# Kernel tuning notes

Hardware: AMD Instinct MI355X
Metric: run time of the kernel (lower is better)

The kernel has to match this reference:

```python
import jax, jax.numpy as jnp
import numpy as np

H, NH, R = 128, 8, 6
NB = 2                  # geometric interaction blocks
BS, L, K = 16, 64, 16   # graphs, blocks/graph, atoms/block
NBLK = BS * L           # 1024 blocks total
N = NBLK * K            # 16384 atoms
E = 262144              # atom-level edges
EB = 512                # block-level edges per graph
CUTOFF = 8.0


def _mha(x, in_w, in_b, out_w, out_b):
    # torch nn.MultiheadAttention (batch_first, eval / no dropout). x: [B,S,H]
    B_, S, _ = x.shape
    qkv = x @ in_w + in_b                     # [B,S,3H]
    q, k, v = jnp.split(qkv, 3, axis=-1)
    dh = H // NH
    q = q.reshape(B_, S, NH, dh)
    k = k.reshape(B_, S, NH, dh)
    v = v.reshape(B_, S, NH, dh)
    scores = jnp.einsum('bind,bjnd->bnij', q, k) / np.sqrt(dh).astype(np.float32)
    attn = jax.nn.softmax(scores, axis=-1)
    o = jnp.einsum('bnij,bjnd->bind', attn, v).reshape(B_, S, H)
    return o @ out_w + out_b


def _forward(A, atom_positions, B_types, coords, edge_index, block_edges,
             emb_atom, emb_pos, emb_block, rbf_freq,
             inter_w1, inter_b1, inter_w2, inter_b2,
             upd_w1, upd_b1, upd_w2, upd_b2,
             edge_w1, edge_b1, edge_w2, edge_b2,
             attn_in_w, attn_in_b, attn_out_w, attn_out_b,
             ln_g, ln_b, fin_w1, fin_b1, fin_w2, fin_b2, fin_w3, fin_b3):
    block_id = jnp.repeat(jnp.arange(NBLK), K)  # uniform K atoms per block
    # atom embedding + position embedding + broadcast block embedding
    x = emb_atom[A] + emb_pos[atom_positions] + emb_block[B_types][block_id]  # [N,H]

    # ---- GeometricAtomProcessor ----
    i, j = edge_index[0], edge_index[1]
    d = jnp.linalg.norm(coords[i] - coords[j], axis=-1)       # [E]
    u = jnp.clip(d / CUTOFF, 1e-3, None)
    # DimeNet envelope, exponent=5 -> p=6: 1/u + a u^5 + b u^6 + c u^7
    env = 1.0 / u - 28.0 * u**5 + 48.0 * u**6 - 21.0 * u**7
    rbf = env[:, None] * jnp.sin(rbf_freq[None, :] * u[:, None])  # [E,R]

    for b in range(NB):
        ef = jnp.concatenate([x[i], x[j], rbf], axis=-1)       # [E,2H+R] gather
        m = jax.nn.silu(ef @ inter_w1[b] + inter_b1[b]) @ inter_w2[b] + inter_b2[b]
        agg = jax.ops.segment_sum(m, i, num_segments=N)        # index_add_ scatter
        ui = jnp.concatenate([x, agg], axis=-1)
        x = jax.nn.silu(ui @ upd_w1[b] + upd_b1[b]) @ upd_w2[b] + upd_b2[b] + x

    # scatter_mean over block_id (uniform blocks -> reshape mean)
    blocks = x.reshape(NBLK, K, H).mean(axis=1).reshape(BS, L, H)

    # ---- per-graph block-edge attention (batched over graphs) ----
    src, dst = block_edges[..., 0], block_edges[..., 1]        # [BS,EB]
    bidx = jnp.arange(BS)[:, None]
    ef = jnp.concatenate([blocks[bidx, src], blocks[bidx, dst]], axis=-1)  # [BS,EB,2H]
    ef = jax.nn.relu(ef @ edge_w1 + edge_b1) @ edge_w2 + edge_b2
    ea = _mha(ef, attn_in_w, attn_in_b, attn_out_w, attn_out_b)            # [BS,EB,H]
    seg = (src + bidx * L).reshape(-1)
    sums = jax.ops.segment_sum(ea.reshape(-1, H), seg, num_segments=NBLK)
    cnt = jax.ops.segment_sum(jnp.ones((BS * EB,), ea.dtype), seg, num_segments=NBLK)
    blocks = blocks + (sums / jnp.maximum(cnt, 1.0)[:, None]).reshape(BS, L, H)

    # ---- block self-attention + mean pool ----
    att = _mha(blocks, attn_in_w, attn_in_b, attn_out_w, attn_out_b)
    g = att.mean(axis=1)                                       # [BS,H]
    mu = g.mean(-1, keepdims=True)
    var = ((g - mu) ** 2).mean(-1, keepdims=True)
    g = (g - mu) / jnp.sqrt(var + 1e-5) * ln_g + ln_b
    h1 = jax.nn.relu(g @ fin_w1 + fin_b1)
    h2 = jax.nn.relu(h1 @ fin_w2 + fin_b2)
    return (h2 @ fin_w3 + fin_b3).squeeze(-1)                  # [BS]


def setup_inputs() -> dict:
    key = jax.random.key(0)
    ks = jax.random.split(key, 40)
    def nrm(k, shape, s=0.05):
        return jax.random.normal(k, shape, jnp.float32) * s
    inp = {}
    inp['A'] = jax.random.randint(ks[0], (N,), 0, 100)
    inp['atom_positions'] = jax.random.randint(ks[1], (N,), 0, 16)
    inp['B_types'] = jax.random.randint(ks[2], (NBLK,), 0, 1000)
    inp['coords'] = jax.random.uniform(ks[3], (N, 3), jnp.float32, 0.0, 20.0)
    inp['edge_index'] = jax.random.randint(ks[4], (2, E), 0, N)
    inp['block_edges'] = jax.random.randint(ks[5], (BS, EB, 2), 0, L)
    inp['emb_atom'] = nrm(ks[6], (100, H), 0.5)
    inp['emb_pos'] = nrm(ks[7], (16, H), 0.5)
    inp['emb_block'] = nrm(ks[8], (1000, H), 0.5)
    inp['rbf_freq'] = (jnp.arange(1, R + 1, dtype=jnp.float32) * np.pi)
    inp['inter_w1'] = nrm(ks[9], (NB, 2 * H + R, H))
    inp['inter_b1'] = jnp.zeros((NB, H), jnp.float32)
    inp['inter_w2'] = nrm(ks[10], (NB, H, H))
    inp['inter_b2'] = jnp.zeros((NB, H), jnp.float32)
    inp['upd_w1'] = nrm(ks[11], (NB, 2 * H, H))
    inp['upd_b1'] = jnp.zeros((NB, H), jnp.float32)
    inp['upd_w2'] = nrm(ks[12], (NB, H, H))
    inp['upd_b2'] = jnp.zeros((NB, H), jnp.float32)
    inp['edge_w1'] = nrm(ks[13], (2 * H, H))
    inp['edge_b1'] = jnp.zeros((H,), jnp.float32)
    inp['edge_w2'] = nrm(ks[14], (H, H))
    inp['edge_b2'] = jnp.zeros((H,), jnp.float32)
    inp['attn_in_w'] = nrm(ks[15], (H, 3 * H))
    inp['attn_in_b'] = jnp.zeros((3 * H,), jnp.float32)
    inp['attn_out_w'] = nrm(ks[16], (H, H))
    inp['attn_out_b'] = jnp.zeros((H,), jnp.float32)
    inp['ln_g'] = jnp.ones((H,), jnp.float32)
    inp['ln_b'] = jnp.zeros((H,), jnp.float32)
    inp['fin_w1'] = nrm(ks[17], (H, H))
    inp['fin_b1'] = jnp.zeros((H,), jnp.float32)
    inp['fin_w2'] = nrm(ks[18], (H, H))
    inp['fin_b2'] = jnp.zeros((H,), jnp.float32)
    inp['fin_w3'] = nrm(ks[19], (H, 1))
    inp['fin_b3'] = jnp.zeros((1,), jnp.float32)
    return inp


def reference(A, atom_positions, B_types, coords, edge_index, block_edges,
              emb_atom, emb_pos, emb_block, rbf_freq,
              inter_w1, inter_b1, inter_w2, inter_b2,
              upd_w1, upd_b1, upd_w2, upd_b2,
              edge_w1, edge_b1, edge_w2, edge_b2,
              attn_in_w, attn_in_b, attn_out_w, attn_out_b,
              ln_g, ln_b, fin_w1, fin_b1, fin_w2, fin_b2, fin_w3, fin_b3):
    return _forward(A, atom_positions, B_types, coords, edge_index, block_edges,
                    emb_atom, emb_pos, emb_block, rbf_freq,
                    inter_w1, inter_b1, inter_w2, inter_b2,
                    upd_w1, upd_b1, upd_w2, upd_b2,
                    edge_w1, edge_b1, edge_w2, edge_b2,
                    attn_in_w, attn_in_b, attn_out_w, attn_out_b,
                    ln_g, ln_b, fin_w1, fin_b1, fin_w2, fin_b2, fin_w3, fin_b3)
```

## Files before the change

kernel.cpp:

```cpp
#include <hip/hip_runtime.h>
#include <math.h>

#define H 128
#define NHD 8
#define DH 16
#define RB 6
#define NBI 2
#define BSG 16
#define LBLK 64
#define KATOM 16
#define NBLKT 1024
#define NA 16384
#define NE 262144
#define EBE 512

__device__ __forceinline__ float fsilu(float v) {
  return v * __builtin_amdgcn_rcpf(1.0f + __expf(-v));
}

typedef short v4s __attribute__((ext_vector_type(4)));
typedef float f32x4 __attribute__((ext_vector_type(4)));

__device__ __forceinline__ short f2bf(float f) {
  union { float f; unsigned u; } v; v.f = f;
  unsigned r = v.u + 0x7fffu + ((v.u >> 16) & 1u);
  return (short)(r >> 16);
}

__device__ __forceinline__ float bf2f(short s) {
  union { unsigned u; float f; } v;
  v.u = ((unsigned)(unsigned short)s) << 16;
  return v.f;
}

#if defined(__has_builtin)
#if __has_builtin(__builtin_amdgcn_mfma_f32_16x16x16bf16_1k)
#define HAVE_MFMA16_1K 1
#endif
#endif

#ifdef HAVE_MFMA16_1K
__device__ __forceinline__ f32x4 mfma16(v4s a, v4s b, f32x4 c) {
  return __builtin_amdgcn_mfma_f32_16x16x16bf16_1k(a, b, c, 0, 0, 0);
}
#else
typedef short v8s __attribute__((ext_vector_type(8)));
__device__ __forceinline__ f32x4 mfma16(v4s a, v4s b, f32x4 c) {
  v8s a8 = {a[0], a[1], a[2], a[3], 0, 0, 0, 0};
  v8s b8 = {b[0], b[1], b[2], b[3], 0, 0, 0, 0};
  return __builtin_amdgcn_mfma_f32_16x16x32_bf16(a8, b8, c, 0, 0, 0);
}
#endif

__global__ __launch_bounds__(256) void k_embed(
    const int* __restrict__ A, const int* __restrict__ apos,
    const int* __restrict__ btypes,
    const float* __restrict__ emb_atom, const float* __restrict__ emb_pos,
    const float* __restrict__ emb_block, float* __restrict__ x)
{
  int idx = blockIdx.x * 256 + threadIdx.x;
  int n = idx >> 7, h = idx & 127;
  x[idx] = emb_atom[A[n] * H + h] + emb_pos[apos[n] * H + h]
         + emb_block[btypes[n >> 4] * H + h];
}

__global__ __launch_bounds__(256) void k_hist(
    const int* __restrict__ ei, int* __restrict__ cnt)
{
  int e = blockIdx.x * 256 + threadIdx.x;
  atomicAdd(&cnt[ei[e]], 1);
}

__global__ __launch_bounds__(1024) void k_scan(
    const int* __restrict__ cnt, int* __restrict__ off,
    int* __restrict__ cur, float* __restrict__ cntf)
{
  __shared__ int ps[1024];
  int t = threadIdx.x;
  int base = t * 16;
  int local[16];
  int s = 0;
  #pragma unroll
  for (int k = 0; k < 16; ++k) { local[k] = s; s += cnt[base + k]; }
  ps[t] = s;
  __syncthreads();
  for (int d = 1; d < 1024; d <<= 1) {
    int v = (t >= d) ? ps[t - d] : 0;
    __syncthreads();
    ps[t] += v;
    __syncthreads();
  }
  int offset = (t == 0) ? 0 : ps[t - 1];
  #pragma unroll
  for (int k = 0; k < 16; ++k) {
    int o = offset + local[k];
    off[base + k] = o;
    cur[base + k] = o;
    cntf[base + k] = (float)cnt[base + k];
  }
  if (t == 1023) off[NA] = offset + s;
}

__global__ __launch_bounds__(256) void k_scatter(
    const int* __restrict__ ei, const int* __restrict__ ej,
    const float* __restrict__ coords, const float* __restrict__ freq,
    int* __restrict__ cur, int* __restrict__ ej_s, float* __restrict__ rbf_s)
{
  int e = blockIdx.x * 256 + threadIdx.x;
  int i = ei[e], j = ej[e];
  int pos = atomicAdd(&cur[i], 1);
  ej_s[pos] = j;
  float dx = coords[i*3+0] - coords[j*3+0];
  float dy = coords[i*3+1] - coords[j*3+1];
  float dz = coords[i*3+2] - coords[j*3+2];
  float d = sqrtf(dx*dx + dy*dy + dz*dz);
  float u = fmaxf(d * 0.125f, 1e-3f);
  float u2 = u*u, u4 = u2*u2, u5 = u4*u, u6 = u5*u, u7 = u6*u;
  float env = 1.0f/u - 28.0f*u5 + 48.0f*u6 - 21.0f*u7;
  #pragma unroll
  for (int r = 0; r < RB; ++r)
    rbf_s[(size_t)pos*RB + r] = env * __sinf(freq[r] * u);
}

__global__ __launch_bounds__(256) void k_bedge_csr(
    const int* __restrict__ bedges, int* __restrict__ blist,
    int* __restrict__ boff, float* __restrict__ ind)
{
  __shared__ int hist[64], offs[65], curs[64];
  int b = blockIdx.x, t = threadIdx.x;
  if (t < 64) hist[t] = 0;
  __syncthreads();
  for (int e = t; e < EBE; e += 256) atomicAdd(&hist[bedges[(b*EBE + e)*2]], 1);
  __syncthreads();
  if (t == 0) {
    offs[0] = 0;
    for (int k = 0; k < 64; ++k) offs[k+1] = offs[k] + hist[k];
  }
  __syncthreads();
  if (t < 64) curs[t] = offs[t];
  __syncthreads();
  for (int e = t; e < EBE; e += 256) {
    int src = bedges[(b*EBE + e)*2];
    int pos = atomicAdd(&curs[src], 1);
    blist[b*EBE + pos] = e;
  }
  if (t < 65) boff[b*65 + t] = offs[t];
  if (t < 64) ind[b*64 + t] = (hist[t] > 0) ? 1.0f : 0.0f;
}

__global__ __launch_bounds__(256) void k_edge_csr(
    const short* __restrict__ P, const short* __restrict__ Q,
    const float* __restrict__ rbf_s, const float* __restrict__ W1c,
    const int* __restrict__ ej_s, const int* __restrict__ off,
    float* __restrict__ Hagg)
{
  __shared__ float w[RB * H];
  for (int idx = threadIdx.x; idx < RB * H; idx += 256) w[idx] = W1c[idx];
  __syncthreads();
  int c4 = threadIdx.x & 31;
  int sub = threadIdx.x >> 5;
  int i = blockIdx.x * 8 + sub;
  int e0 = off[i], e1 = off[i + 1];
  short4 p4 = *(const short4*)&P[(size_t)i * H + c4 * 4];
  float4 pv = { bf2f(p4.x), bf2f(p4.y), bf2f(p4.z), bf2f(p4.w) };
  float4 W0 = *(const float4*)&w[0*H + c4*4];
  float4 W1 = *(const float4*)&w[1*H + c4*4];
  float4 W2 = *(const float4*)&w[2*H + c4*4];
  float4 W3 = *(const float4*)&w[3*H + c4*4];
  float4 W4 = *(const float4*)&w[4*H + c4*4];
  float4 W5 = *(const float4*)&w[5*H + c4*4];
  float4 acc = {0, 0, 0, 0};
  for (int e = e0; e < e1; ++e) {
    int j = ej_s[e];
    short4 q4 = *(const short4*)&Q[(size_t)j * H + c4 * 4];
    float4 qv = { bf2f(q4.x), bf2f(q4.y), bf2f(q4.z), bf2f(q4.w) };
    const float* rb = &rbf_s[(size_t)e * RB];
    float r0 = rb[0], r1 = rb[1], r2 = rb[2], r3 = rb[3], r4 = rb[4], r5 = rb[5];
    float4 v;
    v.x = pv.x + qv.x + r0*W0.x + r1*W1.x + r2*W2.x + r3*W3.x + r4*W4.x + r5*W5.x;
    v.y = pv.y + qv.y + r0*W0.y + r1*W1.y + r2*W2.y + r3*W3.y + r4*W4.y + r5*W5.y;
    v.z = pv.z + qv.z + r0*W0.z + r1*W1.z + r2*W2.z + r3*W3.z + r4*W4.z + r5*W5.z;
    v.w = pv.w + qv.w + r0*W0.w + r1*W1.w + r2*W2.w + r3*W3.w + r4*W4.w + r5*W5.w;
    acc.x += fsilu(v.x);
    acc.y += fsilu(v.y);
    acc.z += fsilu(v.z);
    acc.w += fsilu(v.w);
  }
  *(float4*)&Hagg[(size_t)i * H + c4 * 4] = acc;
}

__global__ __launch_bounds__(128) void k_wprep(
    const float* __restrict__ W2base, const float* __restrict__ U1base,
    const float* __restrict__ b2base, float* __restrict__ bvecbase,
    short* __restrict__ wt_u1base)
{
  int y = blockIdx.y;
  const float* W2 = W2base + (size_t)y * H * H;
  const float* U1 = U1base + (size_t)y * 2 * H * H;
  const float* b2 = b2base + y * H;
  float* bvec = bvecbase + y * H;
  short* wt1 = wt_u1base + (size_t)y * 128 * 256;
  int k = blockIdx.x, c = threadIdx.x;
  const float* U1b = U1 + 128 * H;
  wt1[c * 256 + k] = f2bf(U1[k * H + c]);
  float s = 0.0f;
  for (int t = 0; t < H; ++t) s += W2[k * H + t] * U1b[t * H + c];
  wt1[c * 256 + 128 + k] = f2bf(s);
  if (k == 0) {
    float sb = 0.0f;
    for (int t = 0; t < H; ++t) sb += b2[t] * U1b[t * H + c];
    bvec[c] = sb;
  }
}

__global__ __launch_bounds__(256) void k_tcvt(
    const float* __restrict__ inter_w1, const float* __restrict__ upd_w2,
    const float* __restrict__ edge_w1, const float* __restrict__ edge_w2,
    const float* __restrict__ attn_in_w,
    short* __restrict__ wt_pq, short* __restrict__ wt_u2,
    short* __restrict__ wt_e1, short* __restrict__ wt_e2,
    short* __restrict__ wt_in)
{
  int idx = blockIdx.x * 256 + threadIdx.x;
  {
    int k = idx & 127, col = (idx >> 7) & 127, y = (idx >> 14) & 1, b = idx >> 15;
    wt_pq[idx] = f2bf(inter_w1[((size_t)b*262 + y*128 + k)*128 + col]);
  }
  if (idx < 2*128*128) {
    int k = idx & 127, col = (idx >> 7) & 127, b = idx >> 14;
    wt_u2[idx] = f2bf(upd_w2[((size_t)b*128 + k)*128 + col]);
    wt_e1[idx] = f2bf(edge_w1[((size_t)b*128 + k)*128 + col]);
  }
  if (idx < 128*128) {
    int k = idx & 127, col = idx >> 7;
    wt_e2[idx] = f2bf(edge_w2[(size_t)k*128 + col]);
  }
  if (idx < 384*128) {
    int k = idx & 127, col = idx >> 7;
    wt_in[idx] = f2bf(attn_in_w[(size_t)k*384 + col]);
  }
}

__global__ __launch_bounds__(256) void k_pq_mfma(
    const float* __restrict__ x, const short* __restrict__ WtPQ,
    const float* __restrict__ b1,
    short* __restrict__ P, short* __restrict__ Q)
{
  __shared__ short As[64][136];
  __shared__ short Ws[128][72];
  int tid = threadIdx.x;
  int m0 = blockIdx.x * 64;
  int y = blockIdx.y;
  const short* Wt = WtPQ + (size_t)y * 128 * 128;
  short* C = y ? Q : P;
  for (int idx = tid; idx < 64*32; idx += 256) {
    int r = idx >> 5, c4 = idx & 31;
    float4 v = *(const float4*)&x[(size_t)(m0 + r)*H + c4*4];
    short4 s4 = { f2bf(v.x), f2bf(v.y), f2bf(v.z), f2bf(v.w) };
    *(short4*)&As[r][c4*4] = s4;
  }
  int lane = tid & 63, wv = tid >> 6;
  int c = lane & 15, g = lane >> 4;
  int rowb = wv * 16;
  f32x4 acc[8];
  #pragma unroll
  for (int t = 0; t < 8; ++t) acc[t] = (f32x4){0,0,0,0};
  for (int kc = 0; kc < 2; ++kc) {
    __syncthreads();
    {
      int col = tid >> 1, hh = (tid & 1) * 32;
      const int4* src = (const int4*)&Wt[col*128 + kc*64 + hh];
      int4 a0 = src[0], a1 = src[1], a2 = src[2], a3 = src[3];
      *(int4*)&Ws[col][hh] = a0;      *(int4*)&Ws[col][hh+8] = a1;
      *(int4*)&Ws[col][hh+16] = a2;   *(int4*)&Ws[col][hh+24] = a3;
    }
    __syncthreads();
    #pragma unroll
    for (int ks = 0; ks < 4; ++ks) {
      v4s a = *(const v4s*)&As[rowb + c][kc*64 + ks*16 + g*4];
      #pragma unroll
      for (int ct = 0; ct < 8; ++ct) {
        v4s bf = *(const v4s*)&Ws[ct*16 + c][ks*16 + g*4];
        acc[ct] = mfma16(a, bf, acc[ct]);
      }
    }
  }
  #pragma unroll
  for (int ct = 0; ct < 8; ++ct) {
    int col = ct*16 + c;
    float bb = y ? 0.0f : b1[col];
    #pragma unroll
    for (int r = 0; r < 4; ++r) {
      int row = m0 + rowb + g*4 + r;
      C[(size_t)row*H + col] = f2bf(acc[ct][r] + bb);
    }
  }
}

__global__ __launch_bounds__(256) void k_upd_mfma(
    const float* __restrict__ x, const float* __restrict__ Hagg,
    const short* __restrict__ Wt1,
    const float* __restrict__ b1, const float* __restrict__ bvec,
    const float* __restrict__ cntf,
    const short* __restrict__ Wt2,
    const float* __restrict__ b2,
    float* __restrict__ xout)
{
  __shared__ short As[64][264];
  __shared__ short Ws[128][72];
  __shared__ short Us[64][136];
  int tid = threadIdx.x;
  int m0 = blockIdx.x * 64;
  for (int idx = tid; idx < 64*64; idx += 256) {
    int r = idx >> 6, c4 = idx & 63;
    const float* src = (c4 < 32) ? &x[(size_t)(m0 + r)*H + c4*4]
                                 : &Hagg[(size_t)(m0 + r)*H + (c4-32)*4];
    float4 v = *(const float4*)src;
    short4 s4 = { f2bf(v.x), f2bf(v.y), f2bf(v.z), f2bf(v.w) };
    *(short4*)&As[r][c4*4] = s4;
  }
  int lane = tid & 63, wv = tid >> 6;
  int c = lane & 15, g = lane >> 4;
  int rowb = wv * 16;
  f32x4 acc[8];
  #pragma unroll
  for (int t = 0; t < 8; ++t) acc[t] = (f32x4){0,0,0,0};
  for (int kc = 0; kc < 4; ++kc) {
    __syncthreads();
    {
      int col = tid >> 1, hh = (tid & 1) * 32;
      const int4* src = (const int4*)&Wt1[col*256 + kc*64 + hh];
      int4 a0 = src[0], a1 = src[1], a2 = src[2], a3 = src[3];
      *(int4*)&Ws[col][hh] = a0;      *(int4*)&Ws[col][hh+8] = a1;
      *(int4*)&Ws[col][hh+16] = a2;   *(int4*)&Ws[col][hh+24] = a3;
    }
    __syncthreads();
    #pragma unroll
    for (int ks = 0; ks < 4; ++ks) {
      v4s a = *(const v4s*)&As[rowb + c][kc*64 + ks*16 + g*4];
      #pragma unroll
      for (int ct = 0; ct < 8; ++ct) {
        v4s bf = *(const v4s*)&Ws[ct*16 + c][ks*16 + g*4];
        acc[ct] = mfma16(a, bf, acc[ct]);
      }
    }
  }
  {
    float cr[4];
    #pragma unroll
    for (int r = 0; r < 4; ++r) cr[r] = cntf[m0 + rowb + g*4 + r];
    #pragma unroll
    for (int ct = 0; ct < 8; ++ct) {
      int col = ct*16 + c;
      float bb = b1[col], bv = bvec[col];
      #pragma unroll
      for (int r = 0; r < 4; ++r) {
        float v = acc[ct][r] + bb + bv * cr[r];
        Us[rowb + g*4 + r][col] = f2bf(fsilu(v));
        acc[ct][r] = 0.0f;
      }
    }
  }
  for (int kc = 0; kc < 2; ++kc) {
    __syncthreads();
    {
      int col = tid >> 1, hh = (tid & 1) * 32;
      const int4* src = (const int4*)&Wt2[col*128 + kc*64 + hh];
      int4 a0 = src[0], a1 = src[1], a2 = src[2], a3 = src[3];
      *(int4*)&Ws[col][hh] = a0;      *(int4*)&Ws[col][hh+8] = a1;
      *(int4*)&Ws[col][hh+16] = a2;   *(int4*)&Ws[col][hh+24] = a3;
    }
    __syncthreads();
    #pragma unroll
    for (int ks = 0; ks < 4; ++ks) {
      v4s a = *(const v4s*)&Us[rowb + c][kc*64 + ks*16 + g*4];
      #pragma unroll
      for (int ct = 0; ct < 8; ++ct) {
        v4s bf = *(const v4s*)&Ws[ct*16 + c][ks*16 + g*4];
        acc[ct] = mfma16(a, bf, acc[ct]);
      }
    }
  }
  #pragma unroll
  for (int ct = 0; ct < 8; ++ct) {
    int col = ct*16 + c;
    float bb = b2[col];
    #pragma unroll
    for (int r = 0; r < 4; ++r) {
      int row = m0 + rowb + g*4 + r;
      xout[(size_t)row*H + col] = acc[ct][r] + bb + x[(size_t)row*H + col];
    }
  }
}

__global__ __launch_bounds__(256) void k_eprep_mfma(
    const short* __restrict__ Pb, const short* __restrict__ Qb,
    const int* __restrict__ bedges,
    const short* __restrict__ Wt2e, const float* __restrict__ b2e,
    const short* __restrict__ WtIn, const float* __restrict__ bin,
    float* __restrict__ qkv)
{
  __shared__ short As[64][136];
  __shared__ short Ws[128][72];
  __shared__ short Us[64][136];
  int tid = threadIdx.x;
  int m0 = blockIdx.x * 64;
  for (int idx = tid; idx < 64*32; idx += 256) {
    int r = idx >> 5, c4 = idx & 31;
    int row = m0 + r;
    int g = row >> 9;
    int src = bedges[row*2], dst = bedges[row*2 + 1];
    short4 p4 = *(const short4*)&Pb[(size_t)(g*LBLK + src)*H + c4*4];
    short4 q4 = *(const short4*)&Qb[(size_t)(g*LBLK + dst)*H + c4*4];
    short4 s4;
    s4.x = f2bf(fmaxf(bf2f(p4.x) + bf2f(q4.x), 0.0f));
    s4.y = f2bf(fmaxf(bf2f(p4.y) + bf2f(q4.y), 0.0f));
    s4.z = f2bf(fmaxf(bf2f(p4.z) + bf2f(q4.z), 0.0f));
    s4.w = f2bf(fmaxf(bf2f(p4.w) + bf2f(q4.w), 0.0f));
    *(short4*)&As[r][c4*4] = s4;
  }
  int lane = tid & 63, wv = tid >> 6;
  int c = lane & 15, g = lane >> 4;
  int rowb = wv * 16;
  f32x4 acc[8];
  #pragma unroll
  for (int t = 0; t < 8; ++t) acc[t] = (f32x4){0,0,0,0};
  for (int kc = 0; kc < 2; ++kc) {
    __syncthreads();
    {
      int col = tid >> 1, hh = (tid & 1) * 32;
      const int4* src = (const int4*)&Wt2e[col*128 + kc*64 + hh];
      int4 a0 = src[0], a1 = src[1], a2 = src[2], a3 = src[3];
      *(int4*)&Ws[col][hh] = a0;      *(int4*)&Ws[col][hh+8] = a1;
      *(int4*)&Ws[col][hh+16] = a2;   *(int4*)&Ws[col][hh+24] = a3;
    }
    __syncthreads();
    #pragma unroll
    for (int ks = 0; ks < 4; ++ks) {
      v4s a = *(const v4s*)&As[rowb + c][kc*64 + ks*16 + g*4];
      #pragma unroll
      for (int ct = 0; ct < 8; ++ct) {
        v4s bf = *(const v4s*)&Ws[ct*16 + c][ks*16 + g*4];
        acc[ct] = mfma16(a, bf, acc[ct]);
      }
    }
  }
  #pragma unroll
  for (int ct = 0; ct < 8; ++ct) {
    int col = ct*16 + c;
    float bb = b2e[col];
    #pragma unroll
    for (int r = 0; r < 4; ++r) {
      Us[rowb + g*4 + r][col] = f2bf(acc[ct][r] + bb);
      acc[ct][r] = 0.0f;
    }
  }
  for (int cc = 0; cc < 3; ++cc) {
    for (int kc = 0; kc < 2; ++kc) {
      __syncthreads();
      {
        int col = tid >> 1, hh = (tid & 1) * 32;
        const int4* src = (const int4*)&WtIn[(size_t)(cc*128 + col)*128 + kc*64 + hh];
        int4 a0 = src[0], a1 = src[1], a2 = src[2], a3 = src[3];
        *(int4*)&Ws[col][hh] = a0;      *(int4*)&Ws[col][hh+8] = a1;
        *(int4*)&Ws[col][hh+16] = a2;   *(int4*)&Ws[col][hh+24] = a3;
      }
      __syncthreads();
      #pragma unroll
      for (int ks = 0; ks < 4; ++ks) {
        v4s a = *(const v4s*)&Us[rowb + c][kc*64 + ks*16 + g*4];
        #pragma unroll
        for (int ct = 0; ct < 8; ++ct) {
          v4s bf = *(const v4s*)&Ws[ct*16 + c][ks*16 + g*4];
          acc[ct] = mfma16(a, bf, acc[ct]);
        }
      }
    }
    #pragma unroll
    for (int ct = 0; ct < 8; ++ct) {
      int col = ct*16 + c;
      float bb = bin[cc*128 + col];
      #pragma unroll
      for (int r = 0; r < 4; ++r) {
        int row = m0 + rowb + g*4 + r;
        qkv[(size_t)row*384 + cc*128 + col] = acc[ct][r] + bb;
        acc[ct][r] = 0.0f;
      }
    }
  }
}

__global__ __launch_bounds__(256) void k_bprep(
    const float* __restrict__ bsum, const float* __restrict__ Wout,
    const float* __restrict__ bout, const float* __restrict__ ind,
    const float* __restrict__ blocks,
    const float* __restrict__ Win, const float* __restrict__ bin,
    float* __restrict__ qkv)
{
  __shared__ float As[32][128];
  __shared__ float Ws[16][128];
  __shared__ float Us[32][128];
  int tid = threadIdx.x;
  int m0 = blockIdx.x * 32;
  int chunk = blockIdx.y;
  for (int idx = tid; idx < 32*32; idx += 256) {
    int r = idx >> 5, k4 = idx & 31;
    *(float4*)&As[r][k4*4] = *(const float4*)&bsum[(size_t)(m0 + r)*H + k4*4];
  }
  int rr = tid >> 5;
  int cq = tid & 31;
  float acc[4][4] = {};
  for (int kk0 = 0; kk0 < 128; kk0 += 16) {
    __syncthreads();
    for (int idx = tid; idx < 16*32; idx += 256) {
      int kr = idx >> 5, c4 = idx & 31;
      *(float4*)&Ws[kr][c4*4] = *(const float4*)&Wout[(size_t)(kk0 + kr)*H + c4*4];
    }
    __syncthreads();
    #pragma unroll
    for (int k4 = 0; k4 < 4; ++k4) {
      float4 w0 = *(const float4*)&Ws[k4*4+0][cq*4];
      float4 w1 = *(const float4*)&Ws[k4*4+1][cq*4];
      float4 w2 = *(const float4*)&Ws[k4*4+2][cq*4];
      float4 w3 = *(const float4*)&Ws[k4*4+3][cq*4];
      #pragma unroll
      for (int i = 0; i < 4; ++i) {
        float4 a = *(const float4*)&As[rr + 8*i][kk0 + k4*4];
        acc[i][0] += a.x*w0.x + a.y*w1.x + a.z*w2.x + a.w*w3.x;
        acc[i][1] += a.x*w0.y + a.y*w1.y + a.z*w2.y + a.w*w3.y;
        acc[i][2] += a.x*w0.z + a.y*w1.z + a.z*w2.z + a.w*w3.z;
        acc[i][3] += a.x*w0.w + a.y*w1.w + a.z*w2.w + a.w*w3.w;
      }
    }
  }
  #pragma unroll
  for (int i = 0; i < 4; ++i) {
    int m = m0 + rr + 8*i;
    float bs = ind[m];
    float4 u;
    float* pu = &u.x;
    #pragma unroll
    for (int j = 0; j < 4; ++j) {
      int c = cq*4 + j;
      pu[j] = acc[i][j] + bout[c] * bs + blocks[(size_t)m*H + c];
    }
    *(float4*)&Us[rr + 8*i][cq*4] = u;
    acc[i][0] = 0.0f; acc[i][1] = 0.0f; acc[i][2] = 0.0f; acc[i][3] = 0.0f;
  }
  for (int kk0 = 0; kk0 < 128; kk0 += 16) {
    __syncthreads();
    for (int idx = tid; idx < 16*32; idx += 256) {
      int kr = idx >> 5, c4 = idx & 31;
      *(float4*)&Ws[kr][c4*4] =
          *(const float4*)&Win[(size_t)(kk0 + kr)*384 + chunk*128 + c4*4];
    }
    __syncthreads();
    #pragma unroll
    for (int k4 = 0; k4 < 4; ++k4) {
      float4 w0 = *(const float4*)&Ws[k4*4+0][cq*4];
      float4 w1 = *(const float4*)&Ws[k4*4+1][cq*4];
      float4 w2 = *(const float4*)&Ws[k4*4+2][cq*4];
      float4 w3 = *(const float4*)&Ws[k4*4+3][cq*4];
      #pragma unroll
      for (int i = 0; i < 4; ++i) {
        float4 a = *(const float4*)&Us[rr + 8*i][kk0 + k4*4];
        acc[i][0] += a.x*w0.x + a.y*w1.x + a.z*w2.x + a.w*w3.x;
        acc[i][1] += a.x*w0.y + a.y*w1.y + a.z*w2.y + a.w*w3.y;
        acc[i][2] += a.x*w0.z + a.y*w1.z + a.z*w2.z + a.w*w3.z;
        acc[i][3] += a.x*w0.w + a.y*w1.w + a.z*w2.w + a.w*w3.w;
      }
    }
  }
  #pragma unroll
  for (int i = 0; i < 4; ++i) {
    int m = m0 + rr + 8*i;
    float4 out;
    float* po = &out.x;
    #pragma unroll
    for (int j = 0; j < 4; ++j)
      po[j] = acc[i][j] + bin[chunk*128 + cq*4 + j];
    *(float4*)&qkv[(size_t)m*384 + chunk*128 + cq*4] = out;
  }
}

__global__ __launch_bounds__(256) void k_block_mean(
    const float* __restrict__ x, float* __restrict__ blocks)
{
  int idx = blockIdx.x * 256 + threadIdx.x;
  int nb = idx >> 7, h = idx & 127;
  float s = 0.0f;
  #pragma unroll
  for (int k = 0; k < KATOM; ++k)
    s += x[(size_t)(nb*KATOM + k)*H + h];
  blocks[idx] = s * (1.0f / KATOM);
}

__global__ __launch_bounds__(256) void k_eattn(
    const float* __restrict__ qkv, float* __restrict__ ea)
{
  constexpr int S = EBE;
  constexpr int NR = BSG * NHD * S;
  __shared__ short Ks[S * DH];
  __shared__ short Vt[DH * (S + 4)];
  int rb = blockIdx.x & 7;
  int bh = blockIdx.x >> 3;
  int b = bh >> 3, h = bh & 7;
  const float* base = qkv + (size_t)b * S * 384;
  int tid = threadIdx.x;
  for (int t = tid; t < S * 4; t += 256) {
    int j = t >> 2, q4 = t & 3;
    float4 kv = *(const float4*)(base + (size_t)j * 384 + 128 + h * DH + q4 * 4);
    float4 vv = *(const float4*)(base + (size_t)j * 384 + 256 + h * DH + q4 * 4);
    short* kp = &Ks[j * DH + q4 * 4];
    kp[0] = f2bf(kv.x); kp[1] = f2bf(kv.y); kp[2] = f2bf(kv.z); kp[3] = f2bf(kv.w);
    Vt[(q4*4 + 0) * (S + 4) + j] = f2bf(vv.x);
    Vt[(q4*4 + 1) * (S + 4) + j] = f2bf(vv.y);
    Vt[(q4*4 + 2) * (S + 4) + j] = f2bf(vv.z);
    Vt[(q4*4 + 3) * (S + 4) + j] = f2bf(vv.w);
  }
  __syncthreads();
  int lane = tid & 63, wv = tid >> 6;
  int q = lane & 15;
  int g = lane >> 4;
  int row = rb * 64 + wv * 16 + q;
  float4 qv = *(const float4*)(base + (size_t)row * 384 + h * DH + g * 4);
  v4s qf = { f2bf(qv.x), f2bf(qv.y), f2bf(qv.z), f2bf(qv.w) };
  f32x4 zero = {0.f, 0.f, 0.f, 0.f};
  f32x4 o = zero;
  float m = -1e30f, lsum = 0.0f;
  for (int t = 0; t < S / 16; ++t) {
    v4s ak = *(const v4s*)&Ks[(t * 16 + q) * DH + g * 4];
    f32x4 st = mfma16(ak, qf, zero);
    float tm = fmaxf(fmaxf(st[0], st[1]), fmaxf(st[2], st[3]));
    tm = fmaxf(tm, __shfl_xor(tm, 16));
    tm = fmaxf(tm, __shfl_xor(tm, 32));
    float mn = fmaxf(m, tm);
    float corr = __expf((m - mn) * 0.25f);
    m = mn;
    float p0 = __expf((st[0] - mn) * 0.25f);
    float p1 = __expf((st[1] - mn) * 0.25f);
    float p2 = __expf((st[2] - mn) * 0.25f);
    float p3 = __expf((st[3] - mn) * 0.25f);
    lsum = lsum * corr + ((p0 + p1) + (p2 + p3));
    o[0] *= corr; o[1] *= corr; o[2] *= corr; o[3] *= corr;
    v4s pb = { f2bf(p0), f2bf(p1), f2bf(p2), f2bf(p3) };
    v4s av = *(const v4s*)&Vt[q * (S + 4) + t * 16 + g * 4];
    o = mfma16(av, pb, o);
  }
  float lt = lsum + __shfl_xor(lsum, 16);
  lt += __shfl_xor(lt, 32);
  float inv = 1.0f / lt;
  float4 outv = { o[0]*inv, o[1]*inv, o[2]*inv, o[3]*inv };
  ((float4*)ea)[(size_t)g * NR + (size_t)bh * S + row] = outv;
}

__global__ __launch_bounds__(256) void k_bsum_gather(
    const float* __restrict__ ea, const int* __restrict__ blist,
    const int* __restrict__ boff, float* __restrict__ bsum)
{
  constexpr int NR = BSG * NHD * EBE;
  int idx = blockIdx.x * 256 + threadIdx.x;
  int i = idx >> 5, c4 = idx & 31;
  int b = i >> 6, blk = i & 63;
  int h = c4 >> 2, d4 = c4 & 3;
  int e0 = boff[b*65 + blk], e1 = boff[b*65 + blk + 1];
  const float4* ea4 = (const float4*)ea;
  size_t basein = (size_t)d4 * NR + (size_t)(b*NHD + h) * EBE;
  float4 s = {0, 0, 0, 0};
  for (int e = e0; e < e1; ++e) {
    int srow = blist[b*EBE + e];
    float4 v = ea4[basein + srow];
    s.x += v.x; s.y += v.y; s.z += v.z; s.w += v.w;
  }
  float cnt = (float)(e1 - e0);
  float sc = (cnt > 0.0f) ? (1.0f / cnt) : 0.0f;
  float4 o = {s.x*sc, s.y*sc, s.z*sc, s.w*sc};
  *(float4*)&bsum[(size_t)i*H + c4*4] = o;
}

__global__ __launch_bounds__(256) void k_attnS(
    const float* __restrict__ qkv, float* __restrict__ m2)
{
  __shared__ float Ks[4][LBLK][DH];
  __shared__ float Vs[4][LBLK][DH];
  __shared__ float red[4][LBLK][DH + 1];
  int b = blockIdx.x >> 1, hq = blockIdx.x & 1;
  int tid = threadIdx.x;
  const float* base = qkv + (size_t)b * LBLK * 384;
  for (int t = tid; t < 1024; t += 256) {
    int hl = t >> 8, j = (t >> 2) & 63, d4 = t & 3;
    int h = hq*4 + hl;
    *(float4*)&Ks[hl][j][d4*4] = *(const float4*)(base + (size_t)j*384 + 128 + h*DH + d4*4);
    *(float4*)&Vs[hl][j][d4*4] = *(const float4*)(base + (size_t)j*384 + 256 + h*DH + d4*4);
  }
  __syncthreads();
  int hl = tid >> 6, s = tid & 63;
  int h = hq*4 + hl;
  const float4* qp = (const float4*)(base + (size_t)s * 384 + h * DH);
  float4 q0 = qp[0], q1 = qp[1], q2 = qp[2], q3 = qp[3];
  float m = -1e30f, l = 0.0f;
  float4 o0 = {0,0,0,0}, o1 = {0,0,0,0}, o2 = {0,0,0,0}, o3 = {0,0,0,0};
  for (int c0 = 0; c0 < LBLK; c0 += 32) {
    float scv[32];
    float mc = -1e30f;
    #pragma unroll
    for (int j = 0; j < 32; ++j) {
      float4 k0 = *(const float4*)&Ks[hl][c0+j][0];
      float4 k1 = *(const float4*)&Ks[hl][c0+j][4];
      float4 k2 = *(const float4*)&Ks[hl][c0+j][8];
      float4 k3 = *(const float4*)&Ks[hl][c0+j][12];
      float s0 = q0.x*k0.x + q0.y*k0.y + q0.z*k0.z + q0.w*k0.w;
      float s1 = q1.x*k1.x + q1.y*k1.y + q1.z*k1.z + q1.w*k1.w;
      float s2 = q2.x*k2.x + q2.y*k2.y + q2.z*k2.z + q2.w*k2.w;
      float s3 = q3.x*k3.x + q3.y*k3.y + q3.z*k3.z + q3.w*k3.w;
      float sc = (s0 + s1) + (s2 + s3);
      scv[j] = sc;
      mc = fmaxf(mc, sc);
    }
    float mn = fmaxf(m, mc);
    float corr = __expf((m - mn) * 0.25f);
    l *= corr;
    o0.x *= corr; o0.y *= corr; o0.z *= corr; o0.w *= corr;
    o1.x *= corr; o1.y *= corr; o1.z *= corr; o1.w *= corr;
    o2.x *= corr; o2.y *= corr; o2.z *= corr; o2.w *= corr;
    o3.x *= corr; o3.y *= corr; o3.z *= corr; o3.w *= corr;
    m = mn;
    #pragma unroll
    for (int j = 0; j < 32; ++j) {
      float p = __expf((scv[j] - m) * 0.25f);
      l += p;
      float4 v0 = *(const float4*)&Vs[hl][c0+j][0];
      float4 v1 = *(const float4*)&Vs[hl][c0+j][4];
      float4 v2 = *(const float4*)&Vs[hl][c0+j][8];
      float4 v3 = *(const float4*)&Vs[hl][c0+j][12];
      o0.x += p*v0.x; o0.y += p*v0.y; o0.z += p*v0.z; o0.w += p*v0.w;
      o1.x += p*v1.x; o1.y += p*v1.y; o1.z += p*v1.z; o1.w += p*v1.w;
      o2.x += p*v2.x; o2.y += p*v2.y; o2.z += p*v2.z; o2.w += p*v2.w;
      o3.x += p*v3.x; o3.y += p*v3.y; o3.z += p*v3.z; o3.w += p*v3.w;
    }
  }
  float inv = (1.0f / l) * (1.0f / 64.0f);
  float ov[DH] = {o0.x,o0.y,o0.z,o0.w, o1.x,o1.y,o1.z,o1.w,
                  o2.x,o2.y,o2.z,o2.w, o3.x,o3.y,o3.z,o3.w};
  #pragma unroll
  for (int d = 0; d < DH; ++d) red[hl][s][d] = ov[d] * inv;
  __syncthreads();
  if (s < DH) {
    float acc = 0.0f;
    for (int r = 0; r < LBLK; ++r) acc += red[hl][r][s];
    m2[(size_t)b * H + h * DH + s] = acc;
  }
}

__device__ __forceinline__ float bsum128(float v, float* red) {
  int t = threadIdx.x;
  red[t] = v; __syncthreads();
  #pragma unroll
  for (int off = 64; off > 0; off >>= 1) {
    if (t < off) red[t] += red[t + off];
    __syncthreads();
  }
  float s = red[0];
  __syncthreads();
  return s;
}

__global__ __launch_bounds__(128) void k_final(
    const float* __restrict__ m2, const float* __restrict__ out_w,
    const float* __restrict__ out_b, const float* __restrict__ lng,
    const float* __restrict__ lnb, const float* __restrict__ w1,
    const float* __restrict__ b1, const float* __restrict__ w2,
    const float* __restrict__ b2, const float* __restrict__ w3,
    const float* __restrict__ b3, float* __restrict__ out)
{
  __shared__ float buf[128];
  __shared__ float red[128];
  int b = blockIdx.x, t = threadIdx.x;
  buf[t] = m2[b*H + t];
  __syncthreads();
  float g = out_b[t];
  for (int k = 0; k < H; ++k) g += buf[k] * out_w[k*H + t];
  float mu = bsum128(g, red) * (1.0f / H);
  float df = g - mu;
  float var = bsum128(df * df, red) * (1.0f / H);
  float gn = df / sqrtf(var + 1e-5f) * lng[t] + lnb[t];
  __syncthreads();
  buf[t] = gn; __syncthreads();
  float h1 = b1[t];
  for (int k = 0; k < H; ++k) h1 += buf[k] * w1[k*H + t];
  h1 = fmaxf(h1, 0.0f);
  __syncthreads();
  buf[t] = h1; __syncthreads();
  float h2 = b2[t];
  for (int k = 0; k < H; ++k) h2 += buf[k] * w2[k*H + t];
  h2 = fmaxf(h2, 0.0f);
  float tot = bsum128(h2 * w3[t], red);
  if (t == 0) out[b] = tot + b3[0];
}

extern "C" void kernel_launch(void* const* d_in, const int* in_sizes, int n_in,
                              void* d_out, int out_size, void* d_ws, size_t ws_size,
                              hipStream_t stream) {
  (void)in_sizes; (void)n_in; (void)out_size; (void)ws_size;
  const int*   A          = (const int*)d_in[0];
  const int*   apos       = (const int*)d_in[1];
  const int*   btypes     = (const int*)d_in[2];
  const float* coords     = (const float*)d_in[3];
  const int*   edge_index = (const int*)d_in[4];
  const int*   bedges     = (const int*)d_in[5];
  const float* emb_atom   = (const float*)d_in[6];
  const float* emb_pos    = (const float*)d_in[7];
  const float* emb_block  = (const float*)d_in[8];
  const float* rbf_freq   = (const float*)d_in[9];
  const float* inter_w1   = (const float*)d_in[10];
  const float* inter_b1   = (const float*)d_in[11];
  const float* inter_w2   = (const float*)d_in[12];
  const float* inter_b2   = (const float*)d_in[13];
  const float* upd_w1     = (const float*)d_in[14];
  const float* upd_b1     = (const float*)d_in[15];
  const float* upd_w2     = (const float*)d_in[16];
  const float* upd_b2     = (const float*)d_in[17];
  const float* edge_w1    = (const float*)d_in[18];
  const float* edge_b1    = (const float*)d_in[19];
  const float* edge_w2    = (const float*)d_in[20];
  const float* edge_b2    = (const float*)d_in[21];
  const float* attn_in_w  = (const float*)d_in[22];
  const float* attn_in_b  = (const float*)d_in[23];
  const float* attn_out_w = (const float*)d_in[24];
  const float* attn_out_b = (const float*)d_in[25];
  const float* ln_g       = (const float*)d_in[26];
  const float* ln_b       = (const float*)d_in[27];
  const float* fin_w1     = (const float*)d_in[28];
  const float* fin_b1     = (const float*)d_in[29];
  const float* fin_w2     = (const float*)d_in[30];
  const float* fin_b2     = (const float*)d_in[31];
  const float* fin_w3     = (const float*)d_in[32];
  const float* fin_b3     = (const float*)d_in[33];
  float* out = (float*)d_out;

  float* ws = (float*)d_ws;
  float* x      = ws + 0;
  short* P      = (short*)(ws + 2097152);
  short* Q      = (short*)(ws + 4194304);
  float* Hagg   = ws + 6291456;
  float* rbf_s  = ws + 8388608;
  float* cntf   = ws + 9961472;
  float* blocks = ws + 9977856;
  short* Pb     = (short*)(ws + 10108928);
  short* Qb     = (short*)(ws + 10240000);
  float* qkv    = ws + 12468224;
  float* bsum   = ws + 15613952;
  float* ind    = ws + 15746048;
  float* m2     = ws + 15747072;
  int* blist    = (int*)(ws + 15749120);
  int* boff     = (int*)(ws + 15757312);
  int* ej_s   = (int*)(ws + 10371072);
  int* off    = (int*)(ws + 10371072 + 262144);
  int* cur    = (int*)(ws + 10371072 + 278784);
  int* cnt    = (int*)(ws + 10371072 + 295168);
  float* bvec = ws + 10371072 + 311552;
  short* wt_pq = (short*)(ws + 16777216);
  short* wt_u1 = (short*)(ws + 16777216 + 32768);
  short* wt_u2 = (short*)(ws + 16777216 + 65536);
  short* wt_e1 = (short*)(ws + 16777216 + 81920);
  short* wt_e2 = (short*)(ws + 16777216 + 98304);
  short* wt_in = (short*)(ws + 16777216 + 106496);
  float* ea     = ws + 10371072;

  const int* ei = edge_index;
  const int* ej = edge_index + NE;

  (void)hipMemsetAsync(cnt, 0, NA * sizeof(int), stream);
  k_hist<<<NE/256, 256, 0, stream>>>(ei, cnt);
  k_scan<<<1, 1024, 0, stream>>>(cnt, off, cur, cntf);
  k_scatter<<<NE/256, 256, 0, stream>>>(ei, ej, coords, rbf_freq, cur, ej_s, rbf_s);
  k_bedge_csr<<<BSG, 256, 0, stream>>>(bedges, blist, boff, ind);
  k_wprep<<<dim3(128, 2), 128, 0, stream>>>(inter_w2, upd_w1, inter_b2, bvec, wt_u1);
  k_tcvt<<<256, 256, 0, stream>>>(inter_w1, upd_w2, edge_w1, edge_w2, attn_in_w,
                                  wt_pq, wt_u2, wt_e1, wt_e2, wt_in);

  k_embed<<<NA*H/256, 256, 0, stream>>>(A, apos, btypes, emb_atom, emb_pos, emb_block, x);

  for (int b = 0; b < NBI; ++b) {
    const float* w1 = inter_w1 + (size_t)b * 262 * H;
    k_pq_mfma<<<dim3(NA/64, 2), 256, 0, stream>>>(
        x, wt_pq + (size_t)b*2*128*128, inter_b1 + b*H, P, Q);
    k_edge_csr<<<NA/8, 256, 0, stream>>>(P, Q, rbf_s, w1 + 256*H, ej_s, off, Hagg);
    k_upd_mfma<<<NA/64, 256, 0, stream>>>(
        x, Hagg, wt_u1 + (size_t)b*128*256, upd_b1 + b*H, bvec + b*H, cntf,
        wt_u2 + (size_t)b*128*128, upd_b2 + b*H, x);
  }

  k_block_mean<<<NBLKT*H/256, 256, 0, stream>>>(x, blocks);
  k_pq_mfma<<<dim3(NBLKT/64, 2), 256, 0, stream>>>(blocks, wt_e1, edge_b1, Pb, Qb);
  k_eprep_mfma<<<BSG*EBE/64, 256, 0, stream>>>(Pb, Qb, bedges, wt_e2, edge_b2,
                                               wt_in, attn_in_b, qkv);
  k_eattn<<<BSG*NHD*(EBE/64), 256, 0, stream>>>(qkv, ea);
  k_bsum_gather<<<NBLKT*32/256, 256, 0, stream>>>(ea, blist, boff, bsum);
  k_bprep<<<dim3(NBLKT/32, 3), 256, 0, stream>>>(bsum, attn_out_w, attn_out_b, ind,
                                                 blocks, attn_in_w, attn_in_b, qkv);
  k_attnS<<<BSG*2, 256, 0, stream>>>(qkv, m2);
  k_final<<<BSG, 128, 0, stream>>>(m2, attn_out_w, attn_out_b, ln_g, ln_b,
                                   fin_w1, fin_b1, fin_w2, fin_b2, fin_w3, fin_b3, out);
}
```

Measured before the change: 398.8 us.

## Fuse embed into PQ GEMM, block mean into update, split edge loop, widen attention blocks

Folds the embedding lookup into the first P/Q GEMM and the block-mean reduction into the last update kernel's epilogue, which removes two launches and a full read of x. The edge aggregation kernel now gives each atom two half-waves that handle alternating edges and combines their sums through shared memory, for more memory-level parallelism per atom. The edge attention kernel processes two query tiles per block, halving the grid. Each of these trades launch and traffic savings for extra complexity and a block-wide sync.

New measurement: 399.8 us. Within noise of the previous version (+0.2%).

```diff
diff --git a/kernel.cpp b/kernel.cpp
--- a/kernel.cpp
+++ b/kernel.cpp
@@ -52,18 +52,6 @@
 }
 #endif
 
-__global__ __launch_bounds__(256) void k_embed(
-    const int* __restrict__ A, const int* __restrict__ apos,
-    const int* __restrict__ btypes,
-    const float* __restrict__ emb_atom, const float* __restrict__ emb_pos,
-    const float* __restrict__ emb_block, float* __restrict__ x)
-{
-  int idx = blockIdx.x * 256 + threadIdx.x;
-  int n = idx >> 7, h = idx & 127;
-  x[idx] = emb_atom[A[n] * H + h] + emb_pos[apos[n] * H + h]
-         + emb_block[btypes[n >> 4] * H + h];
-}
-
 __global__ __launch_bounds__(256) void k_hist(
     const int* __restrict__ ei, int* __restrict__ cnt)
 {
@@ -155,11 +143,13 @@
     float* __restrict__ Hagg)
 {
   __shared__ float w[RB * H];
+  __shared__ float accs[4][H];
   for (int idx = threadIdx.x; idx < RB * H; idx += 256) w[idx] = W1c[idx];
   __syncthreads();
   int c4 = threadIdx.x & 31;
-  int sub = threadIdx.x >> 5;
-  int i = blockIdx.x * 8 + sub;
+  int sp = (threadIdx.x >> 5) & 1;
+  int sub = threadIdx.x >> 6;
+  int i = blockIdx.x * 4 + sub;
   int e0 = off[i], e1 = off[i + 1];
   short4 p4 = *(const short4*)&P[(size_t)i * H + c4 * 4];
   float4 pv = { bf2f(p4.x), bf2f(p4.y), bf2f(p4.z), bf2f(p4.w) };
@@ -170,7 +160,32 @@
   float4 W4 = *(const float4*)&w[4*H + c4*4];
   float4 W5 = *(const float4*)&w[5*H + c4*4];
   float4 acc = {0, 0, 0, 0};
-  for (int e = e0; e < e1; ++e) {
+  int e = e0 + sp;
+  for (; e + 2 < e1; e += 4) {
+    int j0 = ej_s[e], j1 = ej_s[e + 2];
+    short4 qa = *(const short4*)&Q[(size_t)j0 * H + c4 * 4];
+    short4 qb = *(const short4*)&Q[(size_t)j1 * H + c4 * 4];
+    const float* ra = &rbf_s[(size_t)e * RB];
+    const float* rc = &rbf_s[(size_t)(e + 2) * RB];
+    float a0 = ra[0], a1 = ra[1], a2 = ra[2], a3 = ra[3], a4 = ra[4], a5 = ra[5];
+    float b0 = rc[0], b1 = rc[1], b2 = rc[2], b3 = rc[3], b4 = rc[4], b5 = rc[5];
+    float4 qv0 = { bf2f(qa.x), bf2f(qa.y), bf2f(qa.z), bf2f(qa.w) };
+    float4 qv1 = { bf2f(qb.x), bf2f(qb.y), bf2f(qb.z), bf2f(qb.w) };
+    float4 v0, v1;
+    v0.x = pv.x + qv0.x + a0*W0.x + a1*W1.x + a2*W2.x + a3*W3.x + a4*W4.x + a5*W5.x;
+    v0.y = pv.y + qv0.y + a0*W0.y + a1*W1.y + a2*W2.y + a3*W3.y + a4*W4.y + a5*W5.y;
+    v0.z = pv.z + qv0.z + a0*W0.z + a1*W1.z + a2*W2.z + a3*W3.z + a4*W4.z + a5*W5.z;
+    v0.w = pv.w + qv0.w + a0*W0.w + a1*W1.w + a2*W2.w + a3*W3.w + a4*W4.w + a5*W5.w;
+    v1.x = pv.x + qv1.x + b0*W0.x + b1*W1.x + b2*W2.x + b3*W3.x + b4*W4.x + b5*W5.x;
+    v1.y = pv.y + qv1.y + b0*W0.y + b1*W1.y + b2*W2.y + b3*W3.y + b4*W4.y + b5*W5.y;
+    v1.z = pv.z + qv1.z + b0*W0.z + b1*W1.z + b2*W2.z + b3*W3.z + b4*W4.z + b5*W5.z;
+    v1.w = pv.w + qv1.w + b0*W0.w + b1*W1.w + b2*W2.w + b3*W3.w + b4*W4.w + b5*W5.w;
+    acc.x += fsilu(v0.x) + fsilu(v1.x);
+    acc.y += fsilu(v0.y) + fsilu(v1.y);
+    acc.z += fsilu(v0.z) + fsilu(v1.z);
+    acc.w += fsilu(v0.w) + fsilu(v1.w);
+  }
+  if (e < e1) {
     int j = ej_s[e];
     short4 q4 = *(const short4*)&Q[(size_t)j * H + c4 * 4];
     float4 qv = { bf2f(q4.x), bf2f(q4.y), bf2f(q4.z), bf2f(q4.w) };
@@ -181,12 +196,16 @@
     v.y = pv.y + qv.y + r0*W0.y + r1*W1.y + r2*W2.y + r3*W3.y + r4*W4.y + r5*W5.y;
     v.z = pv.z + qv.z + r0*W0.z + r1*W1.z + r2*W2.z + r3*W3.z + r4*W4.z + r5*W5.z;
     v.w = pv.w + qv.w + r0*W0.w + r1*W1.w + r2*W2.w + r3*W3.w + r4*W4.w + r5*W5.w;
-    acc.x += fsilu(v.x);
-    acc.y += fsilu(v.y);
-    acc.z += fsilu(v.z);
-    acc.w += fsilu(v.w);
-  }
-  *(float4*)&Hagg[(size_t)i * H + c4 * 4] = acc;
+    acc.x += fsilu(v.x); acc.y += fsilu(v.y);
+    acc.z += fsilu(v.z); acc.w += fsilu(v.w);
+  }
+  if (sp == 1) *(float4*)&accs[sub][c4*4] = acc;
+  __syncthreads();
+  if (sp == 0) {
+    float4 o = *(const float4*)&accs[sub][c4*4];
+    o.x += acc.x; o.y += acc.y; o.z += acc.z; o.w += acc.w;
+    *(float4*)&Hagg[(size_t)i * H + c4 * 4] = o;
+  }
 }
 
 __global__ __launch_bounds__(128) void k_wprep(
@@ -241,6 +260,71 @@
   }
 }
 
+__global__ __launch_bounds__(256) void k_embed_pq(
+    const int* __restrict__ A, const int* __restrict__ apos,
+    const int* __restrict__ btypes,
+    const float* __restrict__ emb_atom, const float* __restrict__ emb_pos,
+    const float* __restrict__ emb_block,
+    const short* __restrict__ WtPQ, const float* __restrict__ b1,
+    float* __restrict__ x, short* __restrict__ P, short* __restrict__ Q)
+{
+  __shared__ short As[64][136];
+  __shared__ short Ws[128][72];
+  int tid = threadIdx.x;
+  int m0 = blockIdx.x * 64;
+  int y = blockIdx.y;
+  const short* Wt = WtPQ + (size_t)y * 128 * 128;
+  short* C = y ? Q : P;
+  for (int idx = tid; idx < 64*32; idx += 256) {
+    int r = idx >> 5, c4 = idx & 31;
+    int row = m0 + r;
+    int an = A[row], ap = apos[row], bt = btypes[row >> 4];
+    float4 va = *(const float4*)&emb_atom[(size_t)an*H + c4*4];
+    float4 vp = *(const float4*)&emb_pos[(size_t)ap*H + c4*4];
+    float4 vb = *(const float4*)&emb_block[(size_t)bt*H + c4*4];
+    float4 v = { va.x+vp.x+vb.x, va.y+vp.y+vb.y, va.z+vp.z+vb.z, va.w+vp.w+vb.w };
+    if (y == 0) *(float4*)&x[(size_t)row*H + c4*4] = v;
+    short4 s4 = { f2bf(v.x), f2bf(v.y), f2bf(v.z), f2bf(v.w) };
+    *(short4*)&As[r][c4*4] = s4;
+  }
+  int lane = tid & 63, wv = tid >> 6;
+  int c = lane & 15, g = lane >> 4;
+  int rowb = wv * 16;
+  f32x4 acc[8];
+  #pragma unroll
+  for (int t = 0; t < 8; ++t) acc[t] = (f32x4){0,0,0,0};
+  for (int kc = 0; kc < 2; ++kc) {
+    __syncthreads();
+    {
+      int col = tid >> 1, hh = (tid & 1) * 32;
+      const int4* src = (const int4*)&Wt[col*128 + kc*64 + hh];
+      int4 a0 = src[0], a1 = src[1], a2 = src[2], a3 = src[3];
+      *(int4*)&Ws[col][hh] = a0;      *(int4*)&Ws[col][hh+8] = a1;
+      *(int4*)&Ws[col][hh+16] = a2;   *(int4*)&Ws[col][hh+24] = a3;
+    }
+    __syncthreads();
+    #pragma unroll
+    for (int ks = 0; ks < 4; ++ks) {
+      v4s a = *(const v4s*)&As[rowb + c][kc*64 + ks*16 + g*4];
+      #pragma unroll
+      for (int ct = 0; ct < 8; ++ct) {
+        v4s bf = *(const v4s*)&Ws[ct*16 + c][ks*16 + g*4];
+        acc[ct] = mfma16(a, bf, acc[ct]);
+      }
+    }
+  }
+  #pragma unroll
+  for (int ct = 0; ct < 8; ++ct) {
+    int col = ct*16 + c;
+    float bb = y ? 0.0f : b1[col];
+    #pragma unroll
+    for (int r = 0; r < 4; ++r) {
+      int row = m0 + rowb + g*4 + r;
+      C[(size_t)row*H + col] = f2bf(acc[ct][r] + bb);
+    }
+  }
+}
+
 __global__ __launch_bounds__(256) void k_pq_mfma(
     const float* __restrict__ x, const short* __restrict__ WtPQ,
     const float* __restrict__ b1,
@@ -304,7 +388,7 @@
     const float* __restrict__ cntf,
     const short* __restrict__ Wt2,
     const float* __restrict__ b2,
-    float* __restrict__ xout)
+    float* __restrict__ xout, float* __restrict__ blocksOut)
 {
   __shared__ short As[64][264];
   __shared__ short Ws[128][72];
@@ -385,10 +469,19 @@
   for (int ct = 0; ct < 8; ++ct) {
     int col = ct*16 + c;
     float bb = b2[col];
+    float bs = 0.0f;
     #pragma unroll
     for (int r = 0; r < 4; ++r) {
       int row = m0 + rowb + g*4 + r;
-      xout[(size_t)row*H + col] = acc[ct][r] + bb + x[(size_t)row*H + col];
+      float v = acc[ct][r] + bb + x[(size_t)row*H + col];
+      xout[(size_t)row*H + col] = v;
+      bs += v;
+    }
+    if (blocksOut) {
+      bs += __shfl_xor(bs, 16);
+      bs += __shfl_xor(bs, 32);
+      if (g == 0)
+        blocksOut[(size_t)(m0/KATOM + wv)*H + col] = bs * (1.0f / KATOM);
     }
   }
 }
@@ -583,18 +676,6 @@
   }
 }
 
-__global__ __launch_bounds__(256) void k_block_mean(
-    const float* __restrict__ x, float* __restrict__ blocks)
-{
-  int idx = blockIdx.x * 256 + threadIdx.x;
-  int nb = idx >> 7, h = idx & 127;
-  float s = 0.0f;
-  #pragma unroll
-  for (int k = 0; k < KATOM; ++k)
-    s += x[(size_t)(nb*KATOM + k)*H + h];
-  blocks[idx] = s * (1.0f / KATOM);
-}
-
 __global__ __launch_bounds__(256) void k_eattn(
     const float* __restrict__ qkv, float* __restrict__ ea)
 {
@@ -602,8 +683,8 @@
   constexpr int NR = BSG * NHD * S;
   __shared__ short Ks[S * DH];
   __shared__ short Vt[DH * (S + 4)];
-  int rb = blockIdx.x & 7;
-  int bh = blockIdx.x >> 3;
+  int rb = blockIdx.x & 3;
+  int bh = blockIdx.x >> 2;
   int b = bh >> 3, h = bh & 7;
   const float* base = qkv + (size_t)b * S * 384;
   int tid = threadIdx.x;
@@ -622,36 +703,38 @@
   int lane = tid & 63, wv = tid >> 6;
   int q = lane & 15;
   int g = lane >> 4;
-  int row = rb * 64 + wv * 16 + q;
-  float4 qv = *(const float4*)(base + (size_t)row * 384 + h * DH + g * 4);
-  v4s qf = { f2bf(qv.x), f2bf(qv.y), f2bf(qv.z), f2bf(qv.w) };
-  f32x4 zero = {0.f, 0.f, 0.f, 0.f};
-  f32x4 o = zero;
-  float m = -1e30f, lsum = 0.0f;
-  for (int t = 0; t < S / 16; ++t) {
-    v4s ak = *(const v4s*)&Ks[(t * 16 + q) * DH + g * 4];
-    f32x4 st = mfma16(ak, qf, zero);
-    float tm = fmaxf(fmaxf(st[0], st[1]), fmaxf(st[2], st[3]));
-    tm = fmaxf(tm, __shfl_xor(tm, 16));
-    tm = fmaxf(tm, __shfl_xor(tm, 32));
-    float mn = fmaxf(m, tm);
-    float corr = __expf((m - mn) * 0.25f);
-    m = mn;
-    float p0 = __expf((st[0] - mn) * 0.25f);
-    float p1 = __expf((st[1] - mn) * 0.25f);
-    float p2 = __expf((st[2] - mn) * 0.25f);
-    float p3 = __expf((st[3] - mn) * 0.25f);
-    lsum = lsum * corr + ((p0 + p1) + (p2 + p3));
-    o[0] *= corr; o[1] *= corr; o[2] *= corr; o[3] *= corr;
-    v4s pb = { f2bf(p0), f2bf(p1), f2bf(p2), f2bf(p3) };
-    v4s av = *(const v4s*)&Vt[q * (S + 4) + t * 16 + g * 4];
-    o = mfma16(av, pb, o);
-  }
-  float lt = lsum + __shfl_xor(lsum, 16);
-  lt += __shfl_xor(lt, 32);
-  float inv = 1.0f / lt;
-  float4 outv = { o[0]*inv, o[1]*inv, o[2]*inv, o[3]*inv };
-  ((float4*)ea)[(size_t)g * NR + (size_t)bh * S + row] = outv;
+  for (int qs = 0; qs < 2; ++qs) {
+    int row = rb * 128 + qs * 64 + wv * 16 + q;
+    float4 qv = *(const float4*)(base + (size_t)row * 384 + h * DH + g * 4);
+    v4s qf = { f2bf(qv.x), f2bf(qv.y), f2bf(qv.z), f2bf(qv.w) };
+    f32x4 zero = {0.f, 0.f, 0.f, 0.f};
+    f32x4 o = zero;
+    float m = -1e30f, lsum = 0.0f;
+    for (int t = 0; t < S / 16; ++t) {
+      v4s ak = *(const v4s*)&Ks[(t * 16 + q) * DH + g * 4];
+      f32x4 st = mfma16(ak, qf, zero);
+      float tm = fmaxf(fmaxf(st[0], st[1]), fmaxf(st[2], st[3]));
+      tm = fmaxf(tm, __shfl_xor(tm, 16));
+      tm = fmaxf(tm, __shfl_xor(tm, 32));
+      float mn = fmaxf(m, tm);
+      float corr = __expf((m - mn) * 0.25f);
+      m = mn;
+      float p0 = __expf((st[0] - mn) * 0.25f);
+      float p1 = __expf((st[1] - mn) * 0.25f);
+      float p2 = __expf((st[2] - mn) * 0.25f);
+      float p3 = __expf((st[3] - mn) * 0.25f);
+      lsum = lsum * corr + ((p0 + p1) + (p2 + p3));
+      o[0] *= corr; o[1] *= corr; o[2] *= corr; o[3] *= corr;
+      v4s pb = { f2bf(p0), f2bf(p1), f2bf(p2), f2bf(p3) };
+      v4s av = *(const v4s*)&Vt[q * (S + 4) + t * 16 + g * 4];
+      o = mfma16(av, pb, o);
+    }
+    float lt = lsum + __shfl_xor(lsum, 16);
+    lt += __shfl_xor(lt, 32);
+    float inv = 1.0f / lt;
+    float4 outv = { o[0]*inv, o[1]*inv, o[2]*inv, o[3]*inv };
+    ((float4*)ea)[(size_t)g * NR + (size_t)bh * S + row] = outv;
+  }
 }
 
 __global__ __launch_bounds__(256) void k_bsum_gather(
@@ -879,23 +962,27 @@
   k_tcvt<<<256, 256, 0, stream>>>(inter_w1, upd_w2, edge_w1, edge_w2, attn_in_w,
                                   wt_pq, wt_u2, wt_e1, wt_e2, wt_in);
 
-  k_embed<<<NA*H/256, 256, 0, stream>>>(A, apos, btypes, emb_atom, emb_pos, emb_block, x);
-
   for (int b = 0; b < NBI; ++b) {
     const float* w1 = inter_w1 + (size_t)b * 262 * H;
-    k_pq_mfma<<<dim3(NA/64, 2), 256, 0, stream>>>(
-        x, wt_pq + (size_t)b*2*128*128, inter_b1 + b*H, P, Q);
-    k_edge_csr<<<NA/8, 256, 0, stream>>>(P, Q, rbf_s, w1 + 256*H, ej_s, off, Hagg);
+    if (b == 0) {
+      k_embed_pq<<<dim3(NA/64, 2), 256, 0, stream>>>(
+          A, apos, btypes, emb_atom, emb_pos, emb_block,
+          wt_pq, inter_b1, x, P, Q);
+    } else {
+      k_pq_mfma<<<dim3(NA/64, 2), 256, 0, stream>>>(
+          x, wt_pq + (size_t)b*2*128*128, inter_b1 + b*H, P, Q);
+    }
+    k_edge_csr<<<NA/4, 256, 0, stream>>>(P, Q, rbf_s, w1 + 256*H, ej_s, off, Hagg);
     k_upd_mfma<<<NA/64, 256, 0, stream>>>(
         x, Hagg, wt_u1 + (size_t)b*128*256, upd_b1 + b*H, bvec + b*H, cntf,
-        wt_u2 + (size_t)b*128*128, upd_b2 + b*H, x);
-  }
-
-  k_block_mean<<<NBLKT*H/256, 256, 0, stream>>>(x, blocks);
+        wt_u2 + (size_t)b*128*128, upd_b2 + b*H, x,
+        (b == NBI-1) ? blocks : nullptr);
+  }
+
   k_pq_mfma<<<dim3(NBLKT/64, 2), 256, 0, stream>>>(blocks, wt_e1, edge_b1, Pb, Qb);
   k_eprep_mfma<<<BSG*EBE/64, 256, 0, stream>>>(Pb, Qb, bedges, wt_e2, edge_b2,
                                                wt_in, attn_in_b, qkv);
-  k_eattn<<<BSG*NHD*(EBE/64), 256, 0, stream>>>(qkv, ea);
+  k_eattn<<<BSG*NHD*(EBE/128), 256, 0, stream>>>(qkv, ea);
   k_bsum_gather<<<NBLKT*32/256, 256, 0, stream>>>(ea, blist, boff, bsum);
   k_bprep<<<dim3(NBLKT/32, 3), 256, 0, stream>>>(bsum, attn_out_w, attn_out_b, ind,
                                                  blocks, attn_in_w, attn_in_b, qkv);
```
